# Kernel optimization log

Hardware: AMD Instinct MI355X
Metric: run time of the kernel (lower is better)

The kernel has to match this reference:

```python
import math
import jax, jax.numpy as jnp
import numpy as np

B, S, E, H = 2, 2048, 1024, 16
D = E // H  # head_dim = 64
NEG = jnp.float32(-1e9)  # finite stand-in for masked_fill(-inf) to avoid NaN in attn @ V


def setup_inputs() -> dict:
    key = jax.random.key(0)
    ks = jax.random.split(key, 8)
    inp = {
        "query": jax.random.normal(ks[0], (B, S, E), jnp.float32),
        "key": jax.random.normal(ks[1], (B, S, E), jnp.float32),
        "value": jax.random.normal(ks[2], (B, S, E), jnp.float32),
        "Wq": jax.random.normal(ks[3], (E, E), jnp.float32) * 0.02,
        "bq": jnp.zeros((E,), jnp.float32),
        "Wk": jax.random.normal(ks[4], (E, E), jnp.float32) * 0.02,
        "bk": jnp.zeros((E,), jnp.float32),
        "Wv": jax.random.normal(ks[5], (E, E), jnp.float32) * 0.02,
        "bv": jnp.zeros((E,), jnp.float32),
        "pos_bias": jax.random.normal(ks[6], (H, 2 * S - 1), jnp.float32) * 0.02,
    }
    # gather indices: per-head row index [H,1,1] and relative-position index [S,S]
    inp["idx0"] = jnp.arange(H, dtype=jnp.int32).reshape(H, 1, 1)
    rel = np.arange(S)[:, None] - np.arange(S)[None, :] + (S - 1)  # in [0, 2S-2]
    inp["idx1"] = jnp.asarray(rel, jnp.int32)
    # causal boolean mask: True where masked (j > i)
    inp["mask"] = jnp.triu(jnp.ones((S, S), jnp.bool_), k=1)
    return inp


def _split(x):  # [B,S,E] -> [B,H,S,D]
    return x.reshape(B, S, H, D).transpose(0, 2, 1, 3)


def reference(query, key, value, Wq, bq, Wk, bk, Wv, bv, pos_bias, idx0, idx1, mask):
    q = _split(query @ Wq.T + bq)
    k = _split(key @ Wk.T + bk)
    v = _split(value @ Wv.T + bv)
    logits = jnp.einsum("bhqd,bhkd->bhqk", q, k) / math.sqrt(D)  # [B,H,S,S]
    logits = logits + pos_bias[idx0, idx1]  # gather -> [H,S,S], broadcast over B
    logits = jnp.where(mask, NEG, logits)   # masked_fill
    attn = jax.nn.log_softmax(logits, axis=-1)  # module uses LogSoftmax (faithful)
    out = jnp.einsum("bhqk,bhkd->bhqd", attn, v)
    return out.transpose(0, 2, 1, 3).reshape(B, S, E)
```

## Files before the change

kernel.cpp:

```cpp
#include <hip/hip_runtime.h>
#include <math.h>

constexpr int BB = 2;
constexpr int SS = 2048;
constexpr int EE = 1024;
constexpr int HH = 16;
constexpr int DD = 64;

typedef short short8 __attribute__((ext_vector_type(8)));
typedef short short4_t __attribute__((ext_vector_type(4)));
typedef float floatx4 __attribute__((ext_vector_type(4)));
typedef unsigned short ushort_t;

__device__ __forceinline__ ushort_t f2bf(float f) {
    unsigned int u = __float_as_uint(f);
    u += 0x7fffu + ((u >> 16) & 1u);
    return (ushort_t)(u >> 16);
}
__device__ __forceinline__ float bf2f(short s) {
    return __uint_as_float(((unsigned)(ushort_t)s) << 16);
}

__device__ __forceinline__ void gl_lds16(const void* g, void* l) {
    __builtin_amdgcn_global_load_lds(
        (const __attribute__((address_space(1))) void*)g,
        (__attribute__((address_space(3))) void*)l, 16, 0, 0);
}

__global__ __launch_bounds__(256) void repack_all(
    const float* __restrict__ x0, const float* __restrict__ x1, const float* __restrict__ x2,
    const float* __restrict__ w0, const float* __restrict__ w1, const float* __restrict__ w2,
    ushort_t* __restrict__ Xbf, ushort_t* __restrict__ Wbf)
{
    const int idx = blockIdx.x * 256 + threadIdx.x;
    const int row = idx >> 7;
    const int gir = idx & 127;
    const float* src;
    ushort_t* dst;
    int r;
    if (row < 3 * BB * SS) {
        const int z = row >> 12; r = row & (BB * SS - 1);
        src = (z == 0) ? x0 : (z == 1) ? x1 : x2;
        dst = Xbf + (size_t)z * BB * SS * EE;
    } else {
        const int rw = row - 3 * BB * SS;
        const int z = rw >> 10; r = rw & (EE - 1);
        src = (z == 0) ? w0 : (z == 1) ? w1 : w2;
        dst = Wbf + (size_t)z * EE * EE;
    }
    const int blk = gir >> 3, g = gir & 7;
    const int gp = g ^ (r & 7);
    const float* sp = src + (size_t)r * EE + gir * 8;
    float4 a = *(const float4*)sp;
    float4 b = *(const float4*)(sp + 4);
    short8 o;
    o[0] = (short)f2bf(a.x); o[1] = (short)f2bf(a.y); o[2] = (short)f2bf(a.z); o[3] = (short)f2bf(a.w);
    o[4] = (short)f2bf(b.x); o[5] = (short)f2bf(b.y); o[6] = (short)f2bf(b.z); o[7] = (short)f2bf(b.w);
    *(short8*)&dst[(size_t)r * EE + blk * 64 + gp * 8] = o;
}

__global__ __launch_bounds__(256) void proj_kernel(
    const ushort_t* __restrict__ Xall, const ushort_t* __restrict__ Wall,
    const float* __restrict__ bq, const float* __restrict__ bk, const float* __restrict__ bv,
    ushort_t* __restrict__ qb, ushort_t* __restrict__ kbb, ushort_t* __restrict__ vtb)
{
    __shared__ __align__(16) ushort_t Xs[128 * 64];
    __shared__ __align__(16) ushort_t Ws[128 * 64];

    const int z = blockIdx.z;
    const ushort_t* X = Xall + (size_t)z * BB * SS * EE;
    const ushort_t* W = Wall + (size_t)z * EE * EE;
    const float* bias = (z == 0) ? bq : (z == 1) ? bk : bv;

    const int t = threadIdx.x, w = t >> 6, l = t & 63, ln = t & 15, qd = (t >> 4) & 3;
    const int row0 = blockIdx.x * 128;
    const int col0 = blockIdx.y * 128;
    const int wzm = (w & 1) * 64, wzn = (w >> 1) * 64;

    floatx4 acc[4][4];
    #pragma unroll
    for (int i = 0; i < 4; ++i)
        #pragma unroll
        for (int j = 0; j < 4; ++j)
            acc[i][j] = (floatx4){0.f, 0.f, 0.f, 0.f};

    for (int k0 = 0; k0 < EE; k0 += 64) {
        __syncthreads();
        #pragma unroll
        for (int j = 0; j < 4; ++j) {
            const int c = w * 4 + j;
            const int r = c * 8 + (l >> 3);
            gl_lds16(&X[(size_t)(row0 + r) * EE + k0 + (l & 7) * 8], &Xs[c * 512]);
            gl_lds16(&W[(size_t)(col0 + r) * EE + k0 + (l & 7) * 8], &Ws[c * 512]);
        }
        __syncthreads();

        const ushort_t* Am = (z < 2) ? Ws : Xs;
        const ushort_t* Bn = (z < 2) ? Xs : Ws;
        #pragma unroll
        for (int kh = 0; kh < 2; ++kh) {
            const int sw = ((kh * 4 + qd) ^ (ln & 7)) * 8;
            short8 af[4], bfr[4];
            #pragma unroll
            for (int mi = 0; mi < 4; ++mi)
                af[mi] = *(const short8*)&Am[(wzm + mi * 16 + ln) * 64 + sw];
            #pragma unroll
            for (int ni = 0; ni < 4; ++ni)
                bfr[ni] = *(const short8*)&Bn[(wzn + ni * 16 + ln) * 64 + sw];
            #pragma unroll
            for (int mi = 0; mi < 4; ++mi)
                #pragma unroll
                for (int ni = 0; ni < 4; ++ni)
                    acc[mi][ni] = __builtin_amdgcn_mfma_f32_16x16x32_bf16(af[mi], bfr[ni], acc[mi][ni], 0, 0, 0);
        }
    }

    if (z < 2) {
        ushort_t* dst = z ? kbb : qb;
        #pragma unroll
        for (int mi = 0; mi < 4; ++mi) {
            const int o0 = col0 + wzm + mi * 16 + qd * 4;
            const float4 b4 = *(const float4*)&bias[o0];
            const int h = o0 >> 6, d0 = o0 & 63;
            const int g = d0 >> 3, dlow = d0 & 7;
            #pragma unroll
            for (int ni = 0; ni < 4; ++ni) {
                const int s = row0 + wzn + ni * 16 + ln;
                const int b = s >> 11, sr = s & (SS - 1);
                const int gp = g ^ (sr & 7);
                short4_t pk;
                pk[0] = (short)f2bf(acc[mi][ni][0] + b4.x);
                pk[1] = (short)f2bf(acc[mi][ni][1] + b4.y);
                pk[2] = (short)f2bf(acc[mi][ni][2] + b4.z);
                pk[3] = (short)f2bf(acc[mi][ni][3] + b4.w);
                *(short4_t*)&dst[((size_t)((b * HH + h) * SS) + sr) * DD + gp * 8 + dlow] = pk;
            }
        }
    } else {
        #pragma unroll
        for (int mi = 0; mi < 4; ++mi) {
            const int s0 = row0 + wzm + mi * 16 + qd * 4;
            const int b = s0 >> 11, sr0 = s0 & (SS - 1);
            const int sg = (sr0 >> 3) & 7, slow = sr0 & 7;
            #pragma unroll
            for (int ni = 0; ni < 4; ++ni) {
                const int o = col0 + wzn + ni * 16 + ln;
                const int h = o >> 6, d = o & 63;
                const float bvv = bias[o];
                const int gp2 = sg ^ (d & 7);
                short4_t pk;
                pk[0] = (short)f2bf(acc[mi][ni][0] + bvv);
                pk[1] = (short)f2bf(acc[mi][ni][1] + bvv);
                pk[2] = (short)f2bf(acc[mi][ni][2] + bvv);
                pk[3] = (short)f2bf(acc[mi][ni][3] + bvv);
                *(short4_t*)&vtb[((size_t)((b * HH + h) * DD) + d) * SS + (sr0 & ~63) + gp2 * 8 + slow] = pk;
            }
        }
    }
}

__global__ __launch_bounds__(256) void scan_chunks(
    const ushort_t* __restrict__ vtb, float* __restrict__ segsuf)
{
    const int t = threadIdx.x;
    const int d = blockIdx.x * 8 + (t >> 5);
    const int ch = t & 31;
    const int bh = blockIdx.y;
    const ushort_t* src = vtb + ((size_t)(bh * DD + d)) * SS + ch * 64;
    float s = 0.f;
    #pragma unroll
    for (int i = 0; i < 8; ++i) {
        short8 v = *(const short8*)&src[i * 8];
        #pragma unroll
        for (int j = 0; j < 8; ++j) s += bf2f(v[j]);
    }
    #pragma unroll
    for (int delta = 1; delta < 32; delta <<= 1) {
        const float v = __shfl_down(s, delta, 32);
        if (ch + delta < 32) s += v;
    }
    segsuf[((size_t)bh * 33 + ch) * 64 + d] = s;
    if (ch == 31) segsuf[((size_t)bh * 33 + 32) * 64 + d] = 0.f;
}

__global__ __launch_bounds__(256, 4) void attn_kernel(
    const ushort_t* __restrict__ qb, const ushort_t* __restrict__ kbb,
    const ushort_t* __restrict__ vtb, const float* __restrict__ segsuf,
    const float* __restrict__ pb, float* __restrict__ out)
{
    __shared__ __align__(16) ushort_t Ks[2][64 * 64];
    __shared__ __align__(16) ushort_t Vt[2][64 * 64];
    __shared__ float pbL[2048];

    const int t = threadIdx.x, w = t >> 6, ln = t & 15, qd = (t >> 4) & 3;

    const int id = blockIdx.x;
    const int r_ = id & 255, g_ = id >> 8;
    const int bh = r_ & 31, tq = r_ >> 5;
    const int qt = (g_ == 0) ? (31 - tq)
                 : (g_ == 1) ? (23 - tq)
                 : (g_ == 2) ? (8 + tq) : tq;
    const int b = bh >> 4, h = bh & 15, i0 = qt * 64;
    const int r0 = 16 * w;

    const ushort_t* Kbh = kbb + (size_t)bh * SS * DD;
    const ushort_t* Vbh = vtb + (size_t)bh * DD * SS;

    const int srow = t >> 3, scg = t & 7;
    auto stage = [&](int buf, int kt) {
        const int k0 = kt * 64;
        gl_lds16(&Kbh[(size_t)(k0 + srow) * DD + scg * 8],      &Ks[buf][w * 512]);
        gl_lds16(&Kbh[(size_t)(k0 + 32 + srow) * DD + scg * 8], &Ks[buf][2048 + w * 512]);
        gl_lds16(&Vbh[(size_t)srow * SS + k0 + scg * 8],        &Vt[buf][w * 512]);
        gl_lds16(&Vbh[(size_t)(32 + srow) * SS + k0 + scg * 8], &Vt[buf][2048 + w * 512]);
    };

    {
        const float* p = pb + h * (2 * SS - 1) + (SS - 1);
        #pragma unroll
        for (int j = 0; j < 8; ++j) pbL[t * 8 + j] = p[t * 8 + j];
    }

    short8 qf[2];
    #pragma unroll
    for (int kh = 0; kh < 2; ++kh)
        qf[kh] = *(const short8*)&qb[((size_t)bh * SS + i0 + r0 + ln) * DD + (((kh * 4 + qd) ^ (ln & 7)) * 8)];

    stage(0, 0);
    __syncthreads();

    floatx4 accpv[4], accsv[4];
    #pragma unroll
    for (int ct = 0; ct < 4; ++ct) {
        accpv[ct] = (floatx4){0.f, 0.f, 0.f, 0.f};
        accsv[ct] = (floatx4){0.f, 0.f, 0.f, 0.f};
    }
    float psum0 = 0.f, psum1 = 0.f;

    for (int kt = 0; kt <= qt; ++kt) {
        const int k0 = kt * 64;
        const bool diag = (kt == qt);

        if (!diag) {
            stage((kt + 1) & 1, kt + 1);
            asm volatile("s_waitcnt vmcnt(4)" ::: "memory");
        } else {
            asm volatile("s_waitcnt vmcnt(0)" ::: "memory");
        }
        __builtin_amdgcn_s_barrier();

        const ushort_t* KsC = Ks[kt & 1];
        const ushort_t* VtC = Vt[kt & 1];

        floatx4 aq[4];
        #pragma unroll
        for (int mt = 0; mt < 4; ++mt) aq[mt] = (floatx4){0.f, 0.f, 0.f, 0.f};
        #pragma unroll
        for (int kh = 0; kh < 2; ++kh) {
            const int sw = ((kh * 4 + qd) ^ (ln & 7)) * 8;
            #pragma unroll
            for (int mt = 0; mt < 4; ++mt) {
                short8 af = *(const short8*)&KsC[(mt * 16 + ln) * 64 + sw];
                aq[mt] = __builtin_amdgcn_mfma_f32_16x16x32_bf16(af, qf[kh], aq[mt], 0, 0, 0);
            }
        }

        short4_t pfrag[4];
        if (!diag) {
            const int base0 = i0 - k0 + r0 + ln;
            #pragma unroll
            for (int mt = 0; mt < 4; ++mt) {
                const int base = base0 - mt * 16 - qd * 4;
                #pragma unroll
                for (int reg = 0; reg < 4; ++reg) {
                    const float val = aq[mt][reg] * 0.125f + pbL[base - reg];
                    if (reg & 1) psum1 += __expf(val); else psum0 += __expf(val);
                    pfrag[mt][reg] = (short)f2bf(val);
                }
            }
        } else {
            #pragma unroll
            for (int mt = 0; mt < 4; ++mt) {
                const int base = r0 + ln - mt * 16 - qd * 4;
                #pragma unroll
                for (int reg = 0; reg < 4; ++reg) {
                    const int rel = base - reg;
                    const bool ok = rel >= 0;
                    const float val = aq[mt][reg] * 0.125f + pbL[ok ? rel : 0];
                    psum0 += ok ? __expf(val) : 0.f;
                    pfrag[mt][reg] = ok ? (short)f2bf(val) : (short)0;
                }
            }
        }

        const int iloc = r0 + ln;
        #pragma unroll
        for (int kk = 0; kk < 4; ++kk) {
            short4_t uf;
            if (diag) {
                #pragma unroll
                for (int j = 0; j < 4; ++j)
                    uf[j] = (kk * 16 + qd * 4 + j > iloc) ? (short)0x3F80 : (short)0;
            }
            #pragma unroll
            for (int ct = 0; ct < 4; ++ct) {
                const int off = (ct * 16 + ln) * 64 + (((kk * 2 + (qd >> 1)) ^ (ln & 7)) * 8 + (qd & 1) * 4);
                short4_t bfr = *(const short4_t*)&VtC[off];
                accpv[ct] = __builtin_amdgcn_mfma_f32_16x16x16bf16_1k(pfrag[kk], bfr, accpv[ct], 0, 0, 0);
                if (diag)
                    accsv[ct] = __builtin_amdgcn_mfma_f32_16x16x16bf16_1k(uf, bfr, accsv[ct], 0, 0, 0);
            }
        }

        if (!diag)
            __builtin_amdgcn_s_barrier();
    }

    float p = psum0 + psum1;
    p += __shfl_xor(p, 16, 64);
    p += __shfl_xor(p, 32, 64);
    const float lseq = __logf(p);
    float lseR[4];
    #pragma unroll
    for (int reg = 0; reg < 4; ++reg)
        lseR[reg] = __shfl(lseq, qd * 4 + reg, 64);

    const int cmin = qt + 1;
    float tot[4], tail[4];
    #pragma unroll
    for (int ct = 0; ct < 4; ++ct) {
        const int d = ct * 16 + ln;
        tot[ct]  = segsuf[((size_t)bh * 33) * 64 + d];
        tail[ct] = segsuf[((size_t)bh * 33 + cmin) * 64 + d];
    }

    #pragma unroll
    for (int ct = 0; ct < 4; ++ct) {
        const int d = ct * 16 + ln;
        #pragma unroll
        for (int reg = 0; reg < 4; ++reg) {
            const int ig = i0 + r0 + qd * 4 + reg;
            const float o = accpv[ct][reg] - lseR[reg] * tot[ct]
                          - 1e9f * (accsv[ct][reg] + tail[ct]);
            out[((size_t)(b * SS + ig)) * EE + h * DD + d] = o;
        }
    }
}

extern "C" void kernel_launch(void* const* d_in, const int* in_sizes, int n_in,
                              void* d_out, int out_size, void* d_ws, size_t ws_size,
                              hipStream_t stream)
{
    const float* query = (const float*)d_in[0];
    const float* key_  = (const float*)d_in[1];
    const float* value = (const float*)d_in[2];
    const float* Wq = (const float*)d_in[3];
    const float* bq = (const float*)d_in[4];
    const float* Wk = (const float*)d_in[5];
    const float* bk = (const float*)d_in[6];
    const float* Wv = (const float*)d_in[7];
    const float* bv = (const float*)d_in[8];
    const float* pb = (const float*)d_in[9];
    float* out = (float*)d_out;

    float* ws = (float*)d_ws;
    const size_t SZ = (size_t)BB * SS * EE;
    float* segsuf = ws;
    ushort_t* us  = (ushort_t*)(segsuf + (size_t)BB * HH * 33 * DD);
    ushort_t* qbp = us;
    ushort_t* kbp = qbp + SZ;
    ushort_t* vtp = kbp + SZ;
    ushort_t* Xbf = vtp + SZ;
    ushort_t* Wbf = Xbf + 3 * SZ;

    const int ngroups = (3 * BB * SS + 3 * EE) * (EE / 8);
    repack_all<<<ngroups / 256, 256, 0, stream>>>(query, key_, value, Wq, Wk, Wv, Xbf, Wbf);

    proj_kernel<<<dim3(BB * SS / 128, EE / 128, 3), 256, 0, stream>>>(
        Xbf, Wbf, bq, bk, bv, qbp, kbp, vtp);

    scan_chunks<<<dim3(8, BB * HH), 256, 0, stream>>>(vtp, segsuf);

    attn_kernel<<<BB * HH * (SS / 64), 256, 0, stream>>>(
        qbp, kbp, vtp, segsuf, pb, out);
}
```

Baseline: 231.2 us.

## Process 128-row query tiles per block with 32 rows per wave

```diff
diff --git a/kernel.cpp b/kernel.cpp
--- a/kernel.cpp
+++ b/kernel.cpp
@@ -19,6 +19,13 @@
 }
 __device__ __forceinline__ float bf2f(short s) {
     return __uint_as_float(((unsigned)(ushort_t)s) << 16);
+}
+
+__device__ __forceinline__ short4_t pack_bf16x4(float a, float b, float c, float d) {
+    union { unsigned u[2]; short4_t s; } r;
+    asm("v_cvt_pk_bf16_f32 %0, %1, %2" : "=v"(r.u[0]) : "v"(a), "v"(b));
+    asm("v_cvt_pk_bf16_f32 %0, %1, %2" : "=v"(r.u[1]) : "v"(c), "v"(d));
+    return r.s;
 }
 
 __device__ __forceinline__ void gl_lds16(const void* g, void* l) {
@@ -183,7 +190,7 @@
     if (ch == 31) segsuf[((size_t)bh * 33 + 32) * 64 + d] = 0.f;
 }
 
-__global__ __launch_bounds__(256, 4) void attn_kernel(
+__global__ __launch_bounds__(256, 3) void attn_kernel(
     const ushort_t* __restrict__ qb, const ushort_t* __restrict__ kbb,
     const ushort_t* __restrict__ vtb, const float* __restrict__ segsuf,
     const float* __restrict__ pb, float* __restrict__ out)
@@ -196,12 +203,12 @@
 
     const int id = blockIdx.x;
     const int r_ = id & 255, g_ = id >> 8;
-    const int bh = r_ & 31, tq = r_ >> 5;
-    const int qt = (g_ == 0) ? (31 - tq)
-                 : (g_ == 1) ? (23 - tq)
-                 : (g_ == 2) ? (8 + tq) : tq;
-    const int b = bh >> 4, h = bh & 15, i0 = qt * 64;
-    const int r0 = 16 * w;
+    const int bh = r_ & 31, p_ = r_ >> 5;
+    const int qtb = g_ ? p_ : (15 - p_);
+    const int b = bh >> 4, h = bh & 15;
+    const int R = qtb * 128 + w * 32;
+    const int ownkt = 2 * qtb + (w >> 1);
+    const int nkt = 2 * qtb + 2;
 
     const ushort_t* Kbh = kbb + (size_t)bh * SS * DD;
     const ushort_t* Vbh = vtb + (size_t)bh * DD * SS;
@@ -221,27 +228,28 @@
         for (int j = 0; j < 8; ++j) pbL[t * 8 + j] = p[t * 8 + j];
     }
 
-    short8 qf[2];
-    #pragma unroll
-    for (int kh = 0; kh < 2; ++kh)
-        qf[kh] = *(const short8*)&qb[((size_t)bh * SS + i0 + r0 + ln) * DD + (((kh * 4 + qd) ^ (ln & 7)) * 8)];
+    short8 qf[2][2];
+    #pragma unroll
+    for (int hf = 0; hf < 2; ++hf)
+        #pragma unroll
+        for (int kh = 0; kh < 2; ++kh)
+            qf[hf][kh] = *(const short8*)&qb[((size_t)bh * SS + R + hf * 16 + ln) * DD + (((kh * 4 + qd) ^ (ln & 7)) * 8)];
 
     stage(0, 0);
     __syncthreads();
 
-    floatx4 accpv[4], accsv[4];
-    #pragma unroll
-    for (int ct = 0; ct < 4; ++ct) {
-        accpv[ct] = (floatx4){0.f, 0.f, 0.f, 0.f};
-        accsv[ct] = (floatx4){0.f, 0.f, 0.f, 0.f};
-    }
-    float psum0 = 0.f, psum1 = 0.f;
-
-    for (int kt = 0; kt <= qt; ++kt) {
-        const int k0 = kt * 64;
-        const bool diag = (kt == qt);
-
-        if (!diag) {
+    floatx4 accpv[2][4], accsv[2][4];
+    #pragma unroll
+    for (int hf = 0; hf < 2; ++hf)
+        #pragma unroll
+        for (int ct = 0; ct < 4; ++ct) {
+            accpv[hf][ct] = (floatx4){0.f, 0.f, 0.f, 0.f};
+            accsv[hf][ct] = (floatx4){0.f, 0.f, 0.f, 0.f};
+        }
+    float ps[2][2] = {{0.f, 0.f}, {0.f, 0.f}};
+
+    for (int kt = 0; kt < nkt; ++kt) {
+        if (kt + 1 < nkt) {
             stage((kt + 1) & 1, kt + 1);
             asm volatile("s_waitcnt vmcnt(4)" ::: "memory");
         } else {
@@ -249,83 +257,116 @@
         }
         __builtin_amdgcn_s_barrier();
 
-        const ushort_t* KsC = Ks[kt & 1];
-        const ushort_t* VtC = Vt[kt & 1];
-
-        floatx4 aq[4];
-        #pragma unroll
-        for (int mt = 0; mt < 4; ++mt) aq[mt] = (floatx4){0.f, 0.f, 0.f, 0.f};
-        #pragma unroll
-        for (int kh = 0; kh < 2; ++kh) {
-            const int sw = ((kh * 4 + qd) ^ (ln & 7)) * 8;
-            #pragma unroll
-            for (int mt = 0; mt < 4; ++mt) {
-                short8 af = *(const short8*)&KsC[(mt * 16 + ln) * 64 + sw];
-                aq[mt] = __builtin_amdgcn_mfma_f32_16x16x32_bf16(af, qf[kh], aq[mt], 0, 0, 0);
-            }
-        }
-
-        short4_t pfrag[4];
-        if (!diag) {
-            const int base0 = i0 - k0 + r0 + ln;
-            #pragma unroll
-            for (int mt = 0; mt < 4; ++mt) {
-                const int base = base0 - mt * 16 - qd * 4;
-                #pragma unroll
-                for (int reg = 0; reg < 4; ++reg) {
-                    const float val = aq[mt][reg] * 0.125f + pbL[base - reg];
-                    if (reg & 1) psum1 += __expf(val); else psum0 += __expf(val);
-                    pfrag[mt][reg] = (short)f2bf(val);
+        if (kt <= ownkt) {
+            const int k0 = kt * 64;
+            const bool diag = (kt == ownkt);
+            const ushort_t* KsC = Ks[kt & 1];
+            const ushort_t* VtC = Vt[kt & 1];
+
+            floatx4 aq[2][4];
+            #pragma unroll
+            for (int hf = 0; hf < 2; ++hf)
+                #pragma unroll
+                for (int mt = 0; mt < 4; ++mt) aq[hf][mt] = (floatx4){0.f, 0.f, 0.f, 0.f};
+            __builtin_amdgcn_s_setprio(1);
+            #pragma unroll
+            for (int kh = 0; kh < 2; ++kh) {
+                const int sw = ((kh * 4 + qd) ^ (ln & 7)) * 8;
+                #pragma unroll
+                for (int mt = 0; mt < 4; ++mt) {
+                    short8 af = *(const short8*)&KsC[(mt * 16 + ln) * 64 + sw];
+                    aq[0][mt] = __builtin_amdgcn_mfma_f32_16x16x32_bf16(af, qf[0][kh], aq[0][mt], 0, 0, 0);
+                    aq[1][mt] = __builtin_amdgcn_mfma_f32_16x16x32_bf16(af, qf[1][kh], aq[1][mt], 0, 0, 0);
                 }
             }
-        } else {
-            #pragma unroll
-            for (int mt = 0; mt < 4; ++mt) {
-                const int base = r0 + ln - mt * 16 - qd * 4;
-                #pragma unroll
-                for (int reg = 0; reg < 4; ++reg) {
-                    const int rel = base - reg;
-                    const bool ok = rel >= 0;
-                    const float val = aq[mt][reg] * 0.125f + pbL[ok ? rel : 0];
-                    psum0 += ok ? __expf(val) : 0.f;
-                    pfrag[mt][reg] = ok ? (short)f2bf(val) : (short)0;
+            __builtin_amdgcn_s_setprio(0);
+
+            short4_t pfrag[2][4];
+            if (!diag) {
+                #pragma unroll
+                for (int hf = 0; hf < 2; ++hf) {
+                    const int base0 = R - k0 + hf * 16 + ln;
+                    #pragma unroll
+                    for (int mt = 0; mt < 4; ++mt) {
+                        const int base = base0 - mt * 16 - qd * 4;
+                        const float v0 = aq[hf][mt][0] * 0.125f + pbL[base];
+                        const float v1 = aq[hf][mt][1] * 0.125f + pbL[base - 1];
+                        const float v2 = aq[hf][mt][2] * 0.125f + pbL[base - 2];
+                        const float v3 = aq[hf][mt][3] * 0.125f + pbL[base - 3];
+                        ps[hf][0] += __expf(v0) + __expf(v2);
+                        ps[hf][1] += __expf(v1) + __expf(v3);
+                        pfrag[hf][mt] = pack_bf16x4(v0, v1, v2, v3);
+                    }
                 }
-            }
-        }
-
-        const int iloc = r0 + ln;
-        #pragma unroll
-        for (int kk = 0; kk < 4; ++kk) {
-            short4_t uf;
-            if (diag) {
-                #pragma unroll
-                for (int j = 0; j < 4; ++j)
-                    uf[j] = (kk * 16 + qd * 4 + j > iloc) ? (short)0x3F80 : (short)0;
-            }
-            #pragma unroll
-            for (int ct = 0; ct < 4; ++ct) {
-                const int off = (ct * 16 + ln) * 64 + (((kk * 2 + (qd >> 1)) ^ (ln & 7)) * 8 + (qd & 1) * 4);
-                short4_t bfr = *(const short4_t*)&VtC[off];
-                accpv[ct] = __builtin_amdgcn_mfma_f32_16x16x16bf16_1k(pfrag[kk], bfr, accpv[ct], 0, 0, 0);
-                if (diag)
-                    accsv[ct] = __builtin_amdgcn_mfma_f32_16x16x16bf16_1k(uf, bfr, accsv[ct], 0, 0, 0);
-            }
-        }
-
-        if (!diag)
+            } else {
+                const int ilocb = (w & 1) * 32;
+                #pragma unroll
+                for (int hf = 0; hf < 2; ++hf) {
+                    #pragma unroll
+                    for (int mt = 0; mt < 4; ++mt) {
+                        const int base = ilocb + hf * 16 + ln - mt * 16 - qd * 4;
+                        float vv[4];
+                        #pragma unroll
+                        for (int reg = 0; reg < 4; ++reg) {
+                            const int rel = base - reg;
+                            const bool ok = rel >= 0;
+                            const float val = aq[hf][mt][reg] * 0.125f + pbL[ok ? rel : 0];
+                            vv[reg] = ok ? val : 0.f;
+                            ps[hf][0] += ok ? __expf(val) : 0.f;
+                        }
+                        pfrag[hf][mt] = pack_bf16x4(vv[0], vv[1], vv[2], vv[3]);
+                    }
+                }
+            }
+
+            const int iloc0 = (w & 1) * 32 + ln;
+            __builtin_amdgcn_s_setprio(1);
+            #pragma unroll
+            for (int kk = 0; kk < 4; ++kk) {
+                short4_t uf0, uf1;
+                if (diag) {
+                    #pragma unroll
+                    for (int j = 0; j < 4; ++j) {
+                        const int kv = kk * 16 + qd * 4 + j;
+                        uf0[j] = (kv > iloc0)      ? (short)0x3F80 : (short)0;
+                        uf1[j] = (kv > iloc0 + 16) ? (short)0x3F80 : (short)0;
+                    }
+                }
+                #pragma unroll
+                for (int ct = 0; ct < 4; ++ct) {
+                    const int off = (ct * 16 + ln) * 64 + (((kk * 2 + (qd >> 1)) ^ (ln & 7)) * 8 + (qd & 1) * 4);
+                    short4_t bfr = *(const short4_t*)&VtC[off];
+                    accpv[0][ct] = __builtin_amdgcn_mfma_f32_16x16x16bf16_1k(pfrag[0][kk], bfr, accpv[0][ct], 0, 0, 0);
+                    accpv[1][ct] = __builtin_amdgcn_mfma_f32_16x16x16bf16_1k(pfrag[1][kk], bfr, accpv[1][ct], 0, 0, 0);
+                    if (diag) {
+                        accsv[0][ct] = __builtin_amdgcn_mfma_f32_16x16x16bf16_1k(uf0, bfr, accsv[0][ct], 0, 0, 0);
+                        accsv[1][ct] = __builtin_amdgcn_mfma_f32_16x16x16bf16_1k(uf1, bfr, accsv[1][ct], 0, 0, 0);
+                    }
+                }
+            }
+            __builtin_amdgcn_s_setprio(0);
+        }
+
+        if (kt + 1 < nkt)
             __builtin_amdgcn_s_barrier();
     }
 
-    float p = psum0 + psum1;
-    p += __shfl_xor(p, 16, 64);
-    p += __shfl_xor(p, 32, 64);
-    const float lseq = __logf(p);
-    float lseR[4];
-    #pragma unroll
-    for (int reg = 0; reg < 4; ++reg)
-        lseR[reg] = __shfl(lseq, qd * 4 + reg, 64);
-
-    const int cmin = qt + 1;
+    float lseq[2];
+    #pragma unroll
+    for (int hf = 0; hf < 2; ++hf) {
+        float p = ps[hf][0] + ps[hf][1];
+        p += __shfl_xor(p, 16, 64);
+        p += __shfl_xor(p, 32, 64);
+        lseq[hf] = __logf(p);
+    }
+    float lseR[2][4];
+    #pragma unroll
+    for (int hf = 0; hf < 2; ++hf)
+        #pragma unroll
+        for (int reg = 0; reg < 4; ++reg)
+            lseR[hf][reg] = __shfl(lseq[hf], qd * 4 + reg, 64);
+
+    const int cmin = ownkt + 1;
     float tot[4], tail[4];
     #pragma unroll
     for (int ct = 0; ct < 4; ++ct) {
@@ -335,16 +376,18 @@
     }
 
     #pragma unroll
-    for (int ct = 0; ct < 4; ++ct) {
-        const int d = ct * 16 + ln;
-        #pragma unroll
-        for (int reg = 0; reg < 4; ++reg) {
-            const int ig = i0 + r0 + qd * 4 + reg;
-            const float o = accpv[ct][reg] - lseR[reg] * tot[ct]
-                          - 1e9f * (accsv[ct][reg] + tail[ct]);
-            out[((size_t)(b * SS + ig)) * EE + h * DD + d] = o;
-        }
-    }
+    for (int hf = 0; hf < 2; ++hf)
+        #pragma unroll
+        for (int ct = 0; ct < 4; ++ct) {
+            const int d = ct * 16 + ln;
+            #pragma unroll
+            for (int reg = 0; reg < 4; ++reg) {
+                const int ig = R + hf * 16 + qd * 4 + reg;
+                const float o = accpv[hf][ct][reg] - lseR[hf][reg] * tot[ct]
+                              - 1e9f * (accsv[hf][ct][reg] + tail[ct]);
+                out[((size_t)(b * SS + ig)) * EE + h * DD + d] = o;
+            }
+        }
 }
 
 extern "C" void kernel_launch(void* const* d_in, const int* in_sizes, int n_in,
@@ -381,6 +424,6 @@
 
     scan_chunks<<<dim3(8, BB * HH), 256, 0, stream>>>(vtp, segsuf);
 
-    attn_kernel<<<BB * HH * (SS / 64), 256, 0, stream>>>(
+    attn_kernel<<<BB * HH * (SS / 128), 256, 0, stream>>>(
         qbp, kbp, vtp, segsuf, pb, out);
 }
```

Measured after the change: 258.1 us. 11.6% more time.

## Pair complementary causal query tiles per block for balanced attention work

Applied to the files above, without the earlier changes.

```diff
diff --git a/kernel.cpp b/kernel.cpp
--- a/kernel.cpp
+++ b/kernel.cpp
@@ -19,6 +19,13 @@
 }
 __device__ __forceinline__ float bf2f(short s) {
     return __uint_as_float(((unsigned)(ushort_t)s) << 16);
+}
+
+__device__ __forceinline__ short4_t pack_bf16x4(float a, float b, float c, float d) {
+    union { unsigned u[2]; short4_t s; } r;
+    asm("v_cvt_pk_bf16_f32 %0, %1, %2" : "=v"(r.u[0]) : "v"(a), "v"(b));
+    asm("v_cvt_pk_bf16_f32 %0, %1, %2" : "=v"(r.u[1]) : "v"(c), "v"(d));
+    return r.s;
 }
 
 __device__ __forceinline__ void gl_lds16(const void* g, void* l) {
@@ -190,71 +197,104 @@
 {
     __shared__ __align__(16) ushort_t Ks[2][64 * 64];
     __shared__ __align__(16) ushort_t Vt[2][64 * 64];
-    __shared__ float pbL[2048];
 
     const int t = threadIdx.x, w = t >> 6, ln = t & 15, qd = (t >> 4) & 3;
 
     const int id = blockIdx.x;
-    const int r_ = id & 255, g_ = id >> 8;
-    const int bh = r_ & 31, tq = r_ >> 5;
-    const int qt = (g_ == 0) ? (31 - tq)
-                 : (g_ == 1) ? (23 - tq)
-                 : (g_ == 2) ? (8 + tq) : tq;
-    const int b = bh >> 4, h = bh & 15, i0 = qt * 64;
+    const int bh = id & 31, p_ = id >> 5;
+    const int b = bh >> 4, h = bh & 15;
+    const int qtA = 31 - p_, nA = qtA + 1;
+    const int qtB = p_;
     const int r0 = 16 * w;
 
     const ushort_t* Kbh = kbb + (size_t)bh * SS * DD;
     const ushort_t* Vbh = vtb + (size_t)bh * DD * SS;
+    const float* pbh = pb + h * (2 * SS - 1) + (SS - 1);
 
     const int srow = t >> 3, scg = t & 7;
-    auto stage = [&](int buf, int kt) {
-        const int k0 = kt * 64;
+    auto stageg = [&](int buf, int g) {
+        const int k0 = ((g < nA) ? g : (g - nA)) * 64;
         gl_lds16(&Kbh[(size_t)(k0 + srow) * DD + scg * 8],      &Ks[buf][w * 512]);
         gl_lds16(&Kbh[(size_t)(k0 + 32 + srow) * DD + scg * 8], &Ks[buf][2048 + w * 512]);
         gl_lds16(&Vbh[(size_t)srow * SS + k0 + scg * 8],        &Vt[buf][w * 512]);
         gl_lds16(&Vbh[(size_t)(32 + srow) * SS + k0 + scg * 8], &Vt[buf][2048 + w * 512]);
     };
 
-    {
-        const float* p = pb + h * (2 * SS - 1) + (SS - 1);
-        #pragma unroll
-        for (int j = 0; j < 8; ++j) pbL[t * 8 + j] = p[t * 8 + j];
-    }
-
     short8 qf[2];
-    #pragma unroll
-    for (int kh = 0; kh < 2; ++kh)
-        qf[kh] = *(const short8*)&qb[((size_t)bh * SS + i0 + r0 + ln) * DD + (((kh * 4 + qd) ^ (ln & 7)) * 8)];
-
-    stage(0, 0);
+    auto loadQ = [&](int qt) {
+        #pragma unroll
+        for (int kh = 0; kh < 2; ++kh)
+            qf[kh] = *(const short8*)&qb[((size_t)bh * SS + qt * 64 + r0 + ln) * DD + (((kh * 4 + qd) ^ (ln & 7)) * 8)];
+    };
+
+    floatx4 accpv[4], accsv[4];
+    float psum0, psum1;
+    auto resetAcc = [&]() {
+        #pragma unroll
+        for (int ct = 0; ct < 4; ++ct) {
+            accpv[ct] = (floatx4){0.f, 0.f, 0.f, 0.f};
+            accsv[ct] = (floatx4){0.f, 0.f, 0.f, 0.f};
+        }
+        psum0 = 0.f; psum1 = 0.f;
+    };
+
+    auto epilogue = [&](int qt) {
+        float p = psum0 + psum1;
+        p += __shfl_xor(p, 16, 64);
+        p += __shfl_xor(p, 32, 64);
+        const float lseq = __logf(p);
+        float lseR[4];
+        #pragma unroll
+        for (int reg = 0; reg < 4; ++reg)
+            lseR[reg] = __shfl(lseq, qd * 4 + reg, 64);
+        const int cmin = qt + 1;
+        float tot[4], tail[4];
+        #pragma unroll
+        for (int ct = 0; ct < 4; ++ct) {
+            const int d = ct * 16 + ln;
+            tot[ct]  = segsuf[((size_t)bh * 33) * 64 + d];
+            tail[ct] = segsuf[((size_t)bh * 33 + cmin) * 64 + d];
+        }
+        const int i0 = qt * 64;
+        #pragma unroll
+        for (int ct = 0; ct < 4; ++ct) {
+            const int d = ct * 16 + ln;
+            #pragma unroll
+            for (int reg = 0; reg < 4; ++reg) {
+                const int ig = i0 + r0 + qd * 4 + reg;
+                const float o = accpv[ct][reg] - lseR[reg] * tot[ct]
+                              - 1e9f * (accsv[ct][reg] + tail[ct]);
+                out[((size_t)(b * SS + ig)) * EE + h * DD + d] = o;
+            }
+        }
+    };
+
+    loadQ(qtA);
+    resetAcc();
+    stageg(0, 0);
     __syncthreads();
 
-    floatx4 accpv[4], accsv[4];
-    #pragma unroll
-    for (int ct = 0; ct < 4; ++ct) {
-        accpv[ct] = (floatx4){0.f, 0.f, 0.f, 0.f};
-        accsv[ct] = (floatx4){0.f, 0.f, 0.f, 0.f};
-    }
-    float psum0 = 0.f, psum1 = 0.f;
-
-    for (int kt = 0; kt <= qt; ++kt) {
-        const int k0 = kt * 64;
-        const bool diag = (kt == qt);
-
-        if (!diag) {
-            stage((kt + 1) & 1, kt + 1);
+    int qt = qtA, kbase = 0;
+    for (int g = 0; g < 33; ++g) {
+        if (g + 1 < 33) {
+            stageg((g + 1) & 1, g + 1);
             asm volatile("s_waitcnt vmcnt(4)" ::: "memory");
         } else {
             asm volatile("s_waitcnt vmcnt(0)" ::: "memory");
         }
         __builtin_amdgcn_s_barrier();
 
-        const ushort_t* KsC = Ks[kt & 1];
-        const ushort_t* VtC = Vt[kt & 1];
+        const int kt = g - kbase;
+        const int k0 = kt * 64;
+        const bool diag = (kt == qt);
+        const int i0 = qt * 64;
+        const ushort_t* KsC = Ks[g & 1];
+        const ushort_t* VtC = Vt[g & 1];
 
         floatx4 aq[4];
         #pragma unroll
         for (int mt = 0; mt < 4; ++mt) aq[mt] = (floatx4){0.f, 0.f, 0.f, 0.f};
+        __builtin_amdgcn_s_setprio(1);
         #pragma unroll
         for (int kh = 0; kh < 2; ++kh) {
             const int sw = ((kh * 4 + qd) ^ (ln & 7)) * 8;
@@ -264,6 +304,7 @@
                 aq[mt] = __builtin_amdgcn_mfma_f32_16x16x32_bf16(af, qf[kh], aq[mt], 0, 0, 0);
             }
         }
+        __builtin_amdgcn_s_setprio(0);
 
         short4_t pfrag[4];
         if (!diag) {
@@ -271,29 +312,33 @@
             #pragma unroll
             for (int mt = 0; mt < 4; ++mt) {
                 const int base = base0 - mt * 16 - qd * 4;
-                #pragma unroll
-                for (int reg = 0; reg < 4; ++reg) {
-                    const float val = aq[mt][reg] * 0.125f + pbL[base - reg];
-                    if (reg & 1) psum1 += __expf(val); else psum0 += __expf(val);
-                    pfrag[mt][reg] = (short)f2bf(val);
-                }
+                const float v0 = aq[mt][0] * 0.125f + pbh[base];
+                const float v1 = aq[mt][1] * 0.125f + pbh[base - 1];
+                const float v2 = aq[mt][2] * 0.125f + pbh[base - 2];
+                const float v3 = aq[mt][3] * 0.125f + pbh[base - 3];
+                psum0 += __expf(v0) + __expf(v2);
+                psum1 += __expf(v1) + __expf(v3);
+                pfrag[mt] = pack_bf16x4(v0, v1, v2, v3);
             }
         } else {
             #pragma unroll
             for (int mt = 0; mt < 4; ++mt) {
                 const int base = r0 + ln - mt * 16 - qd * 4;
+                float vv[4];
                 #pragma unroll
                 for (int reg = 0; reg < 4; ++reg) {
                     const int rel = base - reg;
                     const bool ok = rel >= 0;
-                    const float val = aq[mt][reg] * 0.125f + pbL[ok ? rel : 0];
+                    const float val = aq[mt][reg] * 0.125f + pbh[ok ? rel : 0];
+                    vv[reg] = ok ? val : 0.f;
                     psum0 += ok ? __expf(val) : 0.f;
-                    pfrag[mt][reg] = ok ? (short)f2bf(val) : (short)0;
                 }
+                pfrag[mt] = pack_bf16x4(vv[0], vv[1], vv[2], vv[3]);
             }
         }
 
         const int iloc = r0 + ln;
+        __builtin_amdgcn_s_setprio(1);
         #pragma unroll
         for (int kk = 0; kk < 4; ++kk) {
             short4_t uf;
@@ -311,38 +356,18 @@
                     accsv[ct] = __builtin_amdgcn_mfma_f32_16x16x16bf16_1k(uf, bfr, accsv[ct], 0, 0, 0);
             }
         }
-
-        if (!diag)
+        __builtin_amdgcn_s_setprio(0);
+
+        if (g + 1 < 33)
             __builtin_amdgcn_s_barrier();
-    }
-
-    float p = psum0 + psum1;
-    p += __shfl_xor(p, 16, 64);
-    p += __shfl_xor(p, 32, 64);
-    const float lseq = __logf(p);
-    float lseR[4];
-    #pragma unroll
-    for (int reg = 0; reg < 4; ++reg)
-        lseR[reg] = __shfl(lseq, qd * 4 + reg, 64);
-
-    const int cmin = qt + 1;
-    float tot[4], tail[4];
-    #pragma unroll
-    for (int ct = 0; ct < 4; ++ct) {
-        const int d = ct * 16 + ln;
-        tot[ct]  = segsuf[((size_t)bh * 33) * 64 + d];
-        tail[ct] = segsuf[((size_t)bh * 33 + cmin) * 64 + d];
-    }
-
-    #pragma unroll
-    for (int ct = 0; ct < 4; ++ct) {
-        const int d = ct * 16 + ln;
-        #pragma unroll
-        for (int reg = 0; reg < 4; ++reg) {
-            const int ig = i0 + r0 + qd * 4 + reg;
-            const float o = accpv[ct][reg] - lseR[reg] * tot[ct]
-                          - 1e9f * (accsv[ct][reg] + tail[ct]);
-            out[((size_t)(b * SS + ig)) * EE + h * DD + d] = o;
+
+        if (diag) {
+            epilogue(qt);
+            if (g + 1 < 33) {
+                loadQ(qtB);
+                resetAcc();
+                qt = qtB; kbase = nA;
+            }
         }
     }
 }
@@ -381,6 +406,6 @@
 
     scan_chunks<<<dim3(8, BB * HH), 256, 0, stream>>>(vtp, segsuf);
 
-    attn_kernel<<<BB * HH * (SS / 64), 256, 0, stream>>>(
+    attn_kernel<<<BB * HH * 16, 256, 0, stream>>>(
         qbp, kbp, vtp, segsuf, pb, out);
 }
```

Result: slower. 261.4 us (+13.1%).
